# Optimization experiments

Measured on AMD Instinct MI355X. Metric: run time of the kernel, lower is better.

Reference implementation:

```python
import jax, jax.numpy as jnp
import numpy as np

ALPHA = 2.0   # snntorch ATan surrogate default
THRESH = 1.0  # snntorch Leaky default threshold

@jax.custom_vjp
def spike(x):
    return (x > 0).astype(x.dtype)

def _spike_fwd(x):
    return spike(x), x

def _spike_bwd(x, g):
    # ATan surrogate gradient: (alpha/2) / (1 + (pi/2 * alpha * x)^2)
    return (g * (ALPHA / 2) / (1 + (jnp.pi / 2 * ALPHA * x) ** 2),)

spike.defvjp(_spike_fwd, _spike_bwd)

def _lif(inp, mem, beta):
    # snntorch Leaky, reset_mechanism='subtract':
    # reset from previous mem (detached), then integrate, then fire
    reset = jax.lax.stop_gradient(spike(mem - THRESH))
    mem = jnp.clip(beta, 0.0, 1.0) * mem + inp - reset * THRESH
    spk = spike(mem - THRESH)
    return spk, mem

def setup_inputs() -> dict:
    key = jax.random.key(0)
    ks = jax.random.split(key, 8)
    V, H, T, B = 32000, 512, 512, 8
    s = 0.02
    inv = 1.0 / np.sqrt(H)
    return {
        "x": jax.random.randint(ks[0], (T, B), 0, V),
        "emb": jax.random.normal(ks[1], (V, H), jnp.float32) * s,
        "pos_emb": jax.random.normal(ks[2], (T, H), jnp.float32) * s,
        "beta1": jnp.full((H,), 0.9, jnp.float32),
        "beta2": jnp.full((H,), 0.9, jnp.float32),
        "beta3": jnp.full((H,), 0.9, jnp.float32),
        "W2": jax.random.normal(ks[3], (H, H), jnp.float32) * inv,
        "b2": jnp.zeros((H,), jnp.float32),
        "W3": jax.random.normal(ks[4], (H, H), jnp.float32) * inv,
        "b3": jnp.zeros((H,), jnp.float32),
        "Wout": jax.random.normal(ks[5], (V, H), jnp.float32) * inv,
        "bout": jnp.zeros((V,), jnp.float32),
    }

def reference(x, emb, pos_emb, beta1, beta2, beta3, W2, b2, W3, b3, Wout, bout):
    T, B = x.shape
    H = emb.shape[1]
    # precompute token + positional embedding for all steps: [T, B, H]
    hid = emb[x] + pos_emb[:, None, :]
    mem0 = jnp.zeros((B, H), emb.dtype)

    def step(carry, h_t):
        m1, m2, m3 = carry
        spk1, m1 = _lif(h_t, m1, beta1)
        h = jax.nn.relu(spk1 @ W2.T + b2)
        spk2, m2 = _lif(h, m2, beta2)
        h = jax.nn.relu(spk2 @ W3.T + b3)
        spk3, m3 = _lif(h, m3, beta3)
        logits = spk3 @ Wout.T + bout  # [B, V]
        return (m1, m2, m3), logits

    _, out = jax.lax.scan(step, (mem0, mem0, mem0), hid)
    return out  # [T, B, V]
```

## Files before the change

kernel.cpp:

```cpp
#include <hip/hip_runtime.h>

#define TT 512
#define BB 8
#define HH 512
#define VV 32000
#define RR (TT * BB)

typedef float v4f __attribute__((ext_vector_type(4)));

__device__ __forceinline__ float clip01(float x) { return fminf(fmaxf(x, 0.0f), 1.0f); }

__global__ void __launch_bounds__(512) snn_scan_kernel(
        const int* __restrict__ x, const float* __restrict__ emb,
        const float* __restrict__ pos,
        const float* __restrict__ beta1, const float* __restrict__ beta2,
        const float* __restrict__ beta3,
        const float* __restrict__ W2, const float* __restrict__ b2,
        const float* __restrict__ W3, const float* __restrict__ b3,
        int* __restrict__ act1, int* __restrict__ act2, int* __restrict__ act3,
        int* __restrict__ cnt3_g) {
    __shared__ int x_lds[TT];
    __shared__ int c1[TT], c2[TT], c3[TT];
    const int b = blockIdx.x;
    const int h = threadIdx.x;

    x_lds[h] = x[h * BB + b];
    c1[h] = 0; c2[h] = 0; c3[h] = 0;
    __syncthreads();

    {
        float bt = clip01(beta1[h]);
        float m = 0.0f;
        for (int t0 = 0; t0 < TT; t0 += 32) {
            float ev[32], pv[32];
#pragma unroll
            for (int u = 0; u < 32; ++u) {
                int xv = x_lds[t0 + u];
                ev[u] = emb[((size_t)xv << 9) + h];
                pv[u] = pos[((t0 + u) << 9) + h];
            }
#pragma unroll
            for (int u = 0; u < 32; ++u) {
                float inp = ev[u] + pv[u];
                float reset = (m > 1.0f) ? 1.0f : 0.0f;
                m = bt * m + inp - reset;
                if (m > 1.0f) {
                    int t = t0 + u;
                    int p = atomicAdd(&c1[t], 1);
                    act1[((t * BB + b) << 9) + p] = h;
                }
            }
        }
    }
    __syncthreads();

    {
        float bh = b2[h];
        float inp0 = fmaxf(bh, 0.0f);
        float bt = clip01(beta2[h]);
        float m = 0.0f;
        for (int t0 = 0; t0 < TT; t0 += 16) {
            int n[16];
#pragma unroll
            for (int u = 0; u < 16; ++u) n[u] = c1[t0 + u];
#pragma unroll
            for (int u = 0; u < 16; ++u) {
                float inp;
                if (n[u] == 0) {
                    inp = inp0;
                } else {
                    float acc = bh;
                    const int* a = act1 + (((t0 + u) * BB + b) << 9);
                    for (int i = 0; i < n[u]; ++i) acc += W2[(h << 9) + a[i]];
                    inp = fmaxf(acc, 0.0f);
                }
                float reset = (m > 1.0f) ? 1.0f : 0.0f;
                m = bt * m + inp - reset;
                if (m > 1.0f) {
                    int t = t0 + u;
                    int p = atomicAdd(&c2[t], 1);
                    act2[((t * BB + b) << 9) + p] = h;
                }
            }
        }
    }
    __syncthreads();

    {
        float bh = b3[h];
        float inp0 = fmaxf(bh, 0.0f);
        float bt = clip01(beta3[h]);
        float m = 0.0f;
        for (int t0 = 0; t0 < TT; t0 += 16) {
            int n[16];
#pragma unroll
            for (int u = 0; u < 16; ++u) n[u] = c2[t0 + u];
#pragma unroll
            for (int u = 0; u < 16; ++u) {
                float inp;
                if (n[u] == 0) {
                    inp = inp0;
                } else {
                    float acc = bh;
                    const int* a = act2 + (((t0 + u) * BB + b) << 9);
                    for (int i = 0; i < n[u]; ++i) acc += W3[(h << 9) + a[i]];
                    inp = fmaxf(acc, 0.0f);
                }
                float reset = (m > 1.0f) ? 1.0f : 0.0f;
                m = bt * m + inp - reset;
                if (m > 1.0f) {
                    int t = t0 + u;
                    int p = atomicAdd(&c3[t], 1);
                    act3[((t * BB + b) << 9) + p] = h;
                }
            }
        }
    }
    __syncthreads();
    cnt3_g[h * BB + b] = c3[h];
}

__global__ void __launch_bounds__(512) out_gemm_kernel(
        const int* __restrict__ cnt, const int* __restrict__ act,
        const float* __restrict__ Wout, const float* __restrict__ bout,
        float* __restrict__ out) {
    int v = blockIdx.x * 2048 + threadIdx.x * 4;
    if (v >= VV) return;
    float4 bv = *(const float4*)(bout + v);
    int r0 = blockIdx.y * 8;
#pragma unroll
    for (int rr = 0; rr < 8; ++rr) {
        int r = r0 + rr;
        int n = cnt[r];
        float4 acc = bv;
        const int* a = act + (r << 9);
        for (int i = 0; i < n; ++i) {
            int k = a[i];
            acc.x += Wout[(size_t)(v + 0) * HH + k];
            acc.y += Wout[(size_t)(v + 1) * HH + k];
            acc.z += Wout[(size_t)(v + 2) * HH + k];
            acc.w += Wout[(size_t)(v + 3) * HH + k];
        }
        v4f st = {acc.x, acc.y, acc.z, acc.w};
        __builtin_nontemporal_store(st, (v4f*)(out + (size_t)r * VV + v));
    }
}

extern "C" void kernel_launch(void* const* d_in, const int* in_sizes, int n_in,
                              void* d_out, int out_size, void* d_ws, size_t ws_size,
                              hipStream_t stream) {
    const int*   x     = (const int*)d_in[0];
    const float* emb   = (const float*)d_in[1];
    const float* pos   = (const float*)d_in[2];
    const float* beta1 = (const float*)d_in[3];
    const float* beta2 = (const float*)d_in[4];
    const float* beta3 = (const float*)d_in[5];
    const float* W2    = (const float*)d_in[6];
    const float* b2    = (const float*)d_in[7];
    const float* W3    = (const float*)d_in[8];
    const float* b3    = (const float*)d_in[9];
    const float* Wout  = (const float*)d_in[10];
    const float* bout  = (const float*)d_in[11];
    float* out = (float*)d_out;

    int* act1 = (int*)d_ws;
    int* act2 = act1 + (size_t)RR * HH;
    int* act3 = act2 + (size_t)RR * HH;
    int* cnt3 = act3 + (size_t)RR * HH;

    snn_scan_kernel<<<BB, HH, 0, stream>>>(x, emb, pos, beta1, beta2, beta3,
                                           W2, b2, W3, b3, act1, act2, act3, cnt3);
    out_gemm_kernel<<<dim3(16, RR / 8), HH, 0, stream>>>(cnt3, act3, Wout, bout, out);
}
```

Before: 683.5 us.

## Restructure output kernel to cover all vocab per block with zero-spike fast path

The output kernel now launches one block per 8 rows, and each thread covers 16 vocab strips, keeping 16 bias vectors in registers. When a row has no spikes it writes the bias directly without looping over weights. The nontemporal stores become ordinary stores. Grid size drops from 8192 to 512 blocks, which lowers parallelism and raises register pressure from the bias array, in exchange for less cnt/act rereading and a cheap path for empty rows.

```diff
diff --git a/kernel.cpp b/kernel.cpp
--- a/kernel.cpp
+++ b/kernel.cpp
@@ -5,8 +5,6 @@
 #define HH 512
 #define VV 32000
 #define RR (TT * BB)
-
-typedef float v4f __attribute__((ext_vector_type(4)));
 
 __device__ __forceinline__ float clip01(float x) { return fminf(fmaxf(x, 0.0f), 1.0f); }
 
@@ -120,29 +118,52 @@
     cnt3_g[h * BB + b] = c3[h];
 }
 
+#define ROWS_PER_BLK 8
+
 __global__ void __launch_bounds__(512) out_gemm_kernel(
         const int* __restrict__ cnt, const int* __restrict__ act,
         const float* __restrict__ Wout, const float* __restrict__ bout,
         float* __restrict__ out) {
-    int v = blockIdx.x * 2048 + threadIdx.x * 4;
-    if (v >= VV) return;
-    float4 bv = *(const float4*)(bout + v);
-    int r0 = blockIdx.y * 8;
+    const int tid = threadIdx.x;
+    const int v0 = tid * 4;
+
+    float4 bv[16];
 #pragma unroll
-    for (int rr = 0; rr < 8; ++rr) {
-        int r = r0 + rr;
-        int n = cnt[r];
-        float4 acc = bv;
-        const int* a = act + (r << 9);
-        for (int i = 0; i < n; ++i) {
-            int k = a[i];
-            acc.x += Wout[(size_t)(v + 0) * HH + k];
-            acc.y += Wout[(size_t)(v + 1) * HH + k];
-            acc.z += Wout[(size_t)(v + 2) * HH + k];
-            acc.w += Wout[(size_t)(v + 3) * HH + k];
+    for (int k = 0; k < 16; ++k) {
+        int v = v0 + k * 2048;
+        if (v < VV) bv[k] = *(const float4*)(bout + v);
+    }
+
+    const int r0 = blockIdx.x * ROWS_PER_BLK;
+#pragma unroll
+    for (int rr = 0; rr < ROWS_PER_BLK; ++rr) {
+        const int r = r0 + rr;
+        const int n = cnt[r];
+        float* __restrict__ orow = out + (size_t)r * VV;
+        if (n == 0) {
+#pragma unroll
+            for (int k = 0; k < 16; ++k) {
+                int v = v0 + k * 2048;
+                if (v < VV) *(float4*)(orow + v) = bv[k];
+            }
+        } else {
+            const int* __restrict__ a = act + (r << 9);
+#pragma unroll
+            for (int k = 0; k < 16; ++k) {
+                int v = v0 + k * 2048;
+                if (v < VV) {
+                    float4 acc = bv[k];
+                    for (int i = 0; i < n; ++i) {
+                        int kk = a[i];
+                        acc.x += Wout[(size_t)(v + 0) * HH + kk];
+                        acc.y += Wout[(size_t)(v + 1) * HH + kk];
+                        acc.z += Wout[(size_t)(v + 2) * HH + kk];
+                        acc.w += Wout[(size_t)(v + 3) * HH + kk];
+                    }
+                    *(float4*)(orow + v) = acc;
+                }
+            }
         }
-        v4f st = {acc.x, acc.y, acc.z, acc.w};
-        __builtin_nontemporal_store(st, (v4f*)(out + (size_t)r * VV + v));
     }
 }
 
@@ -170,5 +191,5 @@
 
     snn_scan_kernel<<<BB, HH, 0, stream>>>(x, emb, pos, beta1, beta2, beta3,
                                            W2, b2, W3, b3, act1, act2, act3, cnt3);
-    out_gemm_kernel<<<dim3(16, RR / 8), HH, 0, stream>>>(cnt3, act3, Wout, bout, out);
+    out_gemm_kernel<<<RR / ROWS_PER_BLK, HH, 0, stream>>>(cnt3, act3, Wout, bout, out);
 }
```

Measured after the change: 687.0 us. No clear change (+0.5%).
